# Optimization experiments

Measured on AMD Instinct MI355X. Metric: run time of the kernel, lower is better.

Reference implementation:

```python
import jax, jax.numpy as jnp
import numpy as np

D_MODEL = 2048
NUM_HEADS = 16
D_KV = D_MODEL // NUM_HEADS
THETA = 10000.0
N_LORA = 4
RANK = 16
BATCH = 2
SEQ = 2048


def setup_inputs() -> dict:
    key = jax.random.key(0)
    ks = jax.random.split(key, 16)
    s = 0.02
    inp = {
        'x': jax.random.normal(ks[0], (BATCH, SEQ, D_MODEL), jnp.float32),
        'lora_start_indices': jnp.sort(jax.random.randint(ks[1], (N_LORA,), 0, BATCH)),
        'Wq': jax.random.normal(ks[2], (D_MODEL, D_MODEL), jnp.float32) * s,
        'Aq': jax.random.normal(ks[3], (N_LORA, RANK, D_MODEL), jnp.float32) * s,
        'Bq': jax.random.normal(ks[4], (N_LORA, D_MODEL, RANK), jnp.float32) * s,
        'Wk': jax.random.normal(ks[5], (D_MODEL, D_MODEL), jnp.float32) * s,
        'Ak': jax.random.normal(ks[6], (N_LORA, RANK, D_MODEL), jnp.float32) * s,
        'Bk': jax.random.normal(ks[7], (N_LORA, D_MODEL, RANK), jnp.float32) * s,
        'Wv': jax.random.normal(ks[8], (D_MODEL, D_MODEL), jnp.float32) * s,
        'Av': jax.random.normal(ks[9], (N_LORA, RANK, D_MODEL), jnp.float32) * s,
        'Bv': jax.random.normal(ks[10], (N_LORA, D_MODEL, RANK), jnp.float32) * s,
        'Wo': jax.random.normal(ks[11], (D_MODEL, D_MODEL), jnp.float32) * s,
        'Ao': jax.random.normal(ks[12], (N_LORA, RANK, D_MODEL), jnp.float32) * s,
        'Bo': jax.random.normal(ks[13], (N_LORA, D_MODEL, RANK), jnp.float32) * s,
    }
    return inp


def _adapter_ids(starts, batch):
    # each batch row b uses the adapter whose start index is the last one <= b
    ids = jnp.searchsorted(starts, jnp.arange(batch), side='right') - 1
    return jnp.clip(ids, 0, starts.shape[0] - 1)


def _multilora(x, ids, W, A, B):
    # x: [b, s, d_in]; W: [d_out, d_in]; A: [L, r, d_in]; B: [L, d_out, r]
    base = jnp.einsum('bsd,od->bso', x, W)
    Ai, Bi = A[ids], B[ids]                       # [b, r, d_in], [b, d_out, r]
    low = jnp.einsum('bsd,brd->bsr', x, Ai)
    return base + jnp.einsum('bsr,bor->bso', low, Bi)


def _rope(x):
    # x: [b, h, s, d]; interleaved pair rotation
    d = x.shape[-1]
    pos = jnp.arange(x.shape[-2], dtype=jnp.float32)
    inv_freq = THETA ** (-jnp.arange(0, d, 2, dtype=jnp.float32) / d)  # [d/2]
    ang = pos[:, None] * inv_freq[None, :]                              # [s, d/2]
    cos, sin = jnp.cos(ang), jnp.sin(ang)
    x1, x2 = x[..., 0::2], x[..., 1::2]
    o1 = x1 * cos - x2 * sin
    o2 = x1 * sin + x2 * cos
    return jnp.stack([o1, o2], axis=-1).reshape(x.shape)


def reference(x, lora_start_indices, Wq, Aq, Bq, Wk, Ak, Bk, Wv, Av, Bv, Wo, Ao, Bo):
    b, s, _ = x.shape
    ids = _adapter_ids(lora_start_indices, b)
    Q = _multilora(x, ids, Wq, Aq, Bq)
    K = _multilora(x, ids, Wk, Ak, Bk)
    V = _multilora(x, ids, Wv, Av, Bv)
    # [b, s, h*d] -> [b, h, s, d]
    split = lambda t: t.reshape(b, s, NUM_HEADS, D_KV).transpose(0, 2, 1, 3)
    Q, K, V = split(Q), split(K), split(V)
    Q, K = _rope(Q), _rope(K)
    scores = jnp.einsum('bhqd,bhkd->bhqk', Q, K) / jnp.sqrt(jnp.asarray(D_KV, x.dtype))
    causal = jnp.tril(jnp.ones((s, s), bool))
    scores = jnp.where(causal, scores, jnp.asarray(-jnp.inf, scores.dtype))
    attn = jax.nn.softmax(scores, axis=-1)
    out = jnp.einsum('bhqk,bhkd->bhqd', attn, V)
    out = out.transpose(0, 2, 1, 3).reshape(b, s, D_MODEL)
    return _multilora(out, ids, Wo, Ao, Bo)
```

## Files before the change

### kernel.cpp

```cpp
#include <hip/hip_runtime.h>

typedef unsigned short u16;
typedef unsigned int   u32;
typedef __bf16  bf16x8 __attribute__((ext_vector_type(8)));
typedef float   f32x4  __attribute__((ext_vector_type(4)));

#define D_MODEL 2048
#define SEQ     2048
#define NHEAD   16
#define DKV     128
#define RANK    16

__device__ __forceinline__ u16 f2b(float f) {
  union { float f; u32 i; } v; v.f = f;
  u32 i = v.i;
  return (u16)((i + 0x7FFFu + ((i >> 16) & 1u)) >> 16);
}
__device__ __forceinline__ u32 pack2(float lo, float hi) {
  return (u32)f2b(lo) | ((u32)f2b(hi) << 16);
}
__device__ __forceinline__ float b2f(u16 u) {
  union { u32 i; float f; } v; v.i = ((u32)u) << 16; return v.f;
}
__device__ __forceinline__ float dot2(u32 xa, u32 aa) {
  return b2f((u16)(xa & 0xFFFFu)) * b2f((u16)(aa & 0xFFFFu)) +
         b2f((u16)(xa >> 16))     * b2f((u16)(aa >> 16));
}
__device__ __forceinline__ int adapter_id(const int* starts, int b) {
  int cnt = 0;
#pragma unroll
  for (int i = 0; i < 4; ++i) cnt += (starts[i] <= b) ? 1 : 0;
  int id = cnt - 1;
  return id < 0 ? 0 : (id > 3 ? 3 : id);
}
__device__ __forceinline__ f32x4 mfma16(bf16x8 a, bf16x8 b, f32x4 c) {
  return __builtin_amdgcn_mfma_f32_16x16x32_bf16(a, b, c, 0, 0, 0);
}
__device__ __forceinline__ void gload16(const u16* g, u16* l) {
  __builtin_amdgcn_global_load_lds(
      (const __attribute__((address_space(1))) void*)g,
      (__attribute__((address_space(3))) void*)l, 16, 0, 0);
}

struct CvtArgs {
  const float* src[13];
  u32 base[14];
};
__global__ __launch_bounds__(256) void k_convert(CvtArgs a, u16* __restrict__ dst) {
  const u32 c = blockIdx.x * 256 + threadIdx.x;
  const u32 el0 = c * 8;
  if (el0 >= a.base[13]) return;
  int t = 0;
#pragma unroll
  for (int i = 1; i < 13; ++i) t += (el0 >= a.base[i]) ? 1 : 0;
  const float* s = a.src[t] + (el0 - a.base[t]);
  const float4 lo = *(const float4*)s;
  const float4 hi = *(const float4*)(s + 4);
  uint4 r;
  r.x = pack2(lo.x, lo.y); r.y = pack2(lo.z, lo.w);
  r.z = pack2(hi.x, hi.y); r.w = pack2(hi.z, hi.w);
  *(uint4*)(dst + el0) = r;
}

template <int TAG>
__global__ __launch_bounds__(256) void k_lowrank(
    const u16* __restrict__ X, const u16* __restrict__ A0,
    const u16* __restrict__ A1, const u16* __restrict__ A2,
    const int* __restrict__ starts, float* __restrict__ low, int nout)
{
  const int m = blockIdx.x;
  const int w = threadIdx.x >> 6, lane = threadIdx.x & 63;
  const int id = adapter_id(starts, m >> 11);
  const u16* Xr = X + (size_t)m * D_MODEL;
  for (int o = w; o < nout; o += 4) {
    const int p = o >> 4, r = o & 15;
    const u16* Ar = (p == 0 ? A0 : p == 1 ? A1 : A2) + (size_t)(id * 16 + r) * D_MODEL;
    float sum = 0.f;
#pragma unroll
    for (int c = 0; c < 4; ++c) {
      const int d = c * 512 + lane * 8;
      const uint4 xv = *(const uint4*)(Xr + d);
      const uint4 av = *(const uint4*)(Ar + d);
      sum += dot2(xv.x, av.x) + dot2(xv.y, av.y) + dot2(xv.z, av.z) + dot2(xv.w, av.w);
    }
#pragma unroll
    for (int off = 32; off >= 1; off >>= 1) sum += __shfl_xor(sum, off, 64);
    if (lane == 0) low[(size_t)m * nout + o] = sum;
  }
}

template <int QKV>
__global__ __launch_bounds__(256, 2) void k_gemm(
    const u16* __restrict__ X,
    const u16* __restrict__ W0, const u16* __restrict__ W1, const u16* __restrict__ W2,
    const u16* __restrict__ B0, const u16* __restrict__ B1, const u16* __restrict__ B2,
    const float* __restrict__ low, int ldlow,
    const int* __restrict__ starts,
    u16* __restrict__ D0, u16* __restrict__ D1, u16* __restrict__ D2,
    float* __restrict__ Df)
{
  __shared__ __attribute__((aligned(16))) u16 At[128 * 64];
  __shared__ __attribute__((aligned(16))) u16 Bt[128 * 64];
  const int tid = threadIdx.x;
  const int w = tid >> 6, lane = tid & 63, quad = lane >> 4, l16 = lane & 15;
  const int wr = w >> 1, wc = w & 1;

  const int nwg = gridDim.x * gridDim.y * gridDim.z;
  const int cpx = nwg >> 3;
  const int lin = blockIdx.x + gridDim.x * (blockIdx.y + gridDim.y * blockIdx.z);
  const int nl  = (lin & 7) * cpx + (lin >> 3);
  const int n0 = (nl & 15) * 128, m0 = ((nl >> 4) & 31) * 128, z = nl >> 9;

  const u16* W  = (z == 0) ? W0 : (z == 1) ? W1 : W2;
  const u16* Bm = (z == 0) ? B0 : (z == 1) ? B1 : B2;
  u16*       D  = (z == 0) ? D0 : (z == 1) ? D1 : D2;
  const int loff = QKV ? z * RANK : 0;
  const int id = adapter_id(starts, m0 >> 11);

  const f32x4 zero4 = {0.f, 0.f, 0.f, 0.f};
  f32x4 acc[4][4];
#pragma unroll
  for (int i = 0; i < 4; ++i)
#pragma unroll
    for (int j = 0; j < 4; ++j) acc[i][j] = zero4;

  const int srow_l = lane >> 3;
  const int sgran  = (lane & 7) ^ srow_l;
  const u16* gA = X + (size_t)(m0 + w * 32 + srow_l) * D_MODEL + sgran * 8;
  const u16* gB = W + (size_t)(n0 + w * 32 + srow_l) * D_MODEL + sgran * 8;
  u16* lA = At + (w * 32) * 64;
  u16* lB = Bt + (w * 32) * 64;

  for (int kt = 0; kt < D_MODEL / 64; ++kt) {
    const int kb = kt * 64;
#pragma unroll
    for (int c = 0; c < 4; ++c)
      gload16(gA + (size_t)(c * 8) * D_MODEL + kb, lA + c * 8 * 64);
#pragma unroll
    for (int c = 0; c < 4; ++c)
      gload16(gB + (size_t)(c * 8) * D_MODEL + kb, lB + c * 8 * 64);
    __syncthreads();
#pragma unroll
    for (int kk = 0; kk < 2; ++kk) {
      bf16x8 af[4], bfr[4];
#pragma unroll
      for (int i = 0; i < 4; ++i) {
        const int row = wr * 64 + i * 16 + l16;
        af[i] = *(const bf16x8*)&At[row * 64 + (((kk * 4 + quad) ^ (l16 & 7)) * 8)];
      }
#pragma unroll
      for (int j = 0; j < 4; ++j) {
        const int row = wc * 64 + j * 16 + l16;
        bfr[j] = *(const bf16x8*)&Bt[row * 64 + (((kk * 4 + quad) ^ (l16 & 7)) * 8)];
      }
#pragma unroll
      for (int i = 0; i < 4; ++i)
#pragma unroll
        for (int j = 0; j < 4; ++j)
          acc[i][j] = mfma16(af[i], bfr[j], acc[i][j]);
    }
    __syncthreads();
  }

  for (int e = tid; e < 4096; e += 256) {
    const int rr = e >> 5, kk = e & 31;
    u16 av = 0, bv = 0;
    if (kk < RANK) {
      av = f2b(low[(size_t)(m0 + rr) * ldlow + loff + kk]);
      bv = Bm[((size_t)id * D_MODEL + n0 + rr) * RANK + kk];
    }
    At[rr * 64 + (kk ^ ((rr & 7) << 3))] = av;
    Bt[rr * 64 + (kk ^ ((rr & 7) << 3))] = bv;
  }
  __syncthreads();
  {
    bf16x8 af[4], bfr[4];
#pragma unroll
    for (int i = 0; i < 4; ++i) {
      const int row = wr * 64 + i * 16 + l16;
      af[i] = *(const bf16x8*)&At[row * 64 + ((quad ^ (l16 & 7)) * 8)];
    }
#pragma unroll
    for (int j = 0; j < 4; ++j) {
      const int row = wc * 64 + j * 16 + l16;
      bfr[j] = *(const bf16x8*)&Bt[row * 64 + ((quad ^ (l16 & 7)) * 8)];
    }
#pragma unroll
    for (int i = 0; i < 4; ++i)
#pragma unroll
      for (int j = 0; j < 4; ++j)
        acc[i][j] = mfma16(af[i], bfr[j], acc[i][j]);
  }

  if (QKV) {
    const float scale = (z == 0) ? 0.08838834764831845f : 1.0f;
    const int ropez = (z <= 1);
#pragma unroll
    for (int i = 0; i < 4; ++i) {
      const int mrow = m0 + wr * 64 + i * 16 + quad * 4;
#pragma unroll
      for (int j = 0; j < 4; ++j) {
        const int col = n0 + wc * 64 + j * 16 + l16;
        const int hh = col >> 7, jj = col & (DKV - 1);
        const float invf = exp2f(-0.20762050593046f * (float)(jj >> 1));
#pragma unroll
        for (int r = 0; r < 4; ++r) {
          const int m = mrow + r;
          const int bb = m >> 11, srw = m & (SEQ - 1);
          float v = acc[i][j][r] * scale;
          if (ropez) {
            float sn, cs;
            __sincosf((float)srw * invf, &sn, &cs);
            const float part = __shfl_xor(v, 1, 64);
            v = (jj & 1) ? (part * sn + v * cs) : (v * cs - part * sn);
          }
          D[(((size_t)(bb * NHEAD + hh)) * SEQ + srw) * DKV + jj] = f2b(v);
        }
      }
    }
  } else {
#pragma unroll
    for (int i = 0; i < 4; ++i) {
      const int mrow = m0 + wr * 64 + i * 16 + quad * 4;
#pragma unroll
      for (int j = 0; j < 4; ++j) {
        const int col = n0 + wc * 64 + j * 16 + l16;
#pragma unroll
        for (int r = 0; r < 4; ++r)
          Df[(size_t)(mrow + r) * D_MODEL + col] = acc[i][j][r];
      }
    }
  }
}

#define M0 8.0f
__global__ __launch_bounds__(256, 3) void k_flash(
    const u16* __restrict__ Q, const u16* __restrict__ K,
    const u16* __restrict__ V, u16* __restrict__ O,
    u16* __restrict__ Opart, float* __restrict__ lpart)
{
  __shared__ __attribute__((aligned(16))) u16 Kl[64 * 136];
  __shared__ __attribute__((aligned(16))) u16 VT[DKV * 72];
  __shared__ __attribute__((aligned(16))) u16 Pl[4 * 16 * 72];
  const int tid = threadIdx.x;
  const int w = tid >> 6, lane = tid & 63, quad = lane >> 4, l16 = lane & 15;
  const int lin = blockIdx.x + 32 * blockIdx.y;
  const int nlb = (lin & 7) * 128 + (lin >> 3);
  const int cid = nlb & 31, bh = nlb >> 5;
  const size_t base = (size_t)bh * SEQ * DKV;
  const u16* Qb = Q + base;
  const u16* Kb = K + base;
  const u16* Vb = V + base;
  const int b = bh >> 4, h = bh & 15;
  u16* Plw = &Pl[w * 1152];
  const f32x4 zero4 = {0.f, 0.f, 0.f, 0.f};

  const int dual = (cid < 16);
  const int nA   = dual ? (cid + 1) : 16;
  const int qtB  = 31 - cid;
  const int n    = dual ? 17 : 16;

  const int krr = tid >> 4;
  const int kc8 = (tid & 15) * 8;
  const int vrp = tid & 31;
  const int vcg = tid >> 5;

  int qt = cid, q0 = cid * 64;
  bf16x8 qa[4];
#pragma unroll
  for (int kc = 0; kc < 4; ++kc)
    qa[kc] = *(const bf16x8*)(Qb + (size_t)(q0 + w * 16 + l16) * DKV + kc * 32 + quad * 8);

  f32x4 oacc[8];
#pragma unroll
  for (int nn = 0; nn < 8; ++nn) oacc[nn] = zero4;
  float lr[4] = {0.f, 0.f, 0.f, 0.f};

  uint4 pk[4], pva[2], pvb[2];
#pragma unroll
  for (int it = 0; it < 4; ++it)
    pk[it] = *(const uint4*)(Kb + (size_t)(krr + it * 16) * DKV + kc8);
#pragma unroll
  for (int it = 0; it < 2; ++it) {
    pva[it] = *(const uint4*)(Vb + (size_t)(2 * vrp)     * DKV + (vcg + it * 8) * 8);
    pvb[it] = *(const uint4*)(Vb + (size_t)(2 * vrp + 1) * DKV + (vcg + it * 8) * 8);
  }

  for (int s = 0; s < n; ++s) {
    if (dual && s == nA) {
      float inv[4];
#pragma unroll
      for (int rg = 0; rg < 4; ++rg) {
        float t = lr[rg];
#pragma unroll
        for (int off = 8; off >= 1; off >>= 1) t += __shfl_xor(t, off, 64);
        inv[rg] = 1.f / t;
        lr[rg] = 0.f;
      }
#pragma unroll
      for (int nn = 0; nn < 8; ++nn) {
        const int col = h * DKV + nn * 16 + l16;
#pragma unroll
        for (int rg = 0; rg < 4; ++rg) {
          const int row = q0 + w * 16 + quad * 4 + rg;
          O[((size_t)b * SEQ + row) * D_MODEL + col] = f2b(oacc[nn][rg] * inv[rg]);
        }
#pragma unroll
        for (int e = 0; e < 4; ++e) oacc[nn][e] = 0.f;
      }
      qt = qtB; q0 = qtB * 64;
#pragma unroll
      for (int kc = 0; kc < 4; ++kc)
        qa[kc] = *(const bf16x8*)(Qb + (size_t)(q0 + w * 16 + l16) * DKV + kc * 32 + quad * 8);
    }
    const int kt = (dual && s >= nA) ? (16 + s - nA) : s;

    __syncthreads();
#pragma unroll
    for (int it = 0; it < 4; ++it)
      *(uint4*)(&Kl[(krr + it * 16) * 136 + kc8]) = pk[it];
#pragma unroll
    for (int it = 0; it < 2; ++it) {
      const int c0 = (vcg + it * 8) * 8;
      const uint4 a = pva[it], c = pvb[it];
      *(u32*)&VT[(c0 + 0) * 72 + 2 * vrp] = (a.x & 0xFFFFu) | (c.x << 16);
      *(u32*)&VT[(c0 + 1) * 72 + 2 * vrp] = (a.x >> 16)     | (c.x & 0xFFFF0000u);
      *(u32*)&VT[(c0 + 2) * 72 + 2 * vrp] = (a.y & 0xFFFFu) | (c.y << 16);
      *(u32*)&VT[(c0 + 3) * 72 + 2 * vrp] = (a.y >> 16)     | (c.y & 0xFFFF0000u);
      *(u32*)&VT[(c0 + 4) * 72 + 2 * vrp] = (a.z & 0xFFFFu) | (c.z << 16);
      *(u32*)&VT[(c0 + 5) * 72 + 2 * vrp] = (a.z >> 16)     | (c.z & 0xFFFF0000u);
      *(u32*)&VT[(c0 + 6) * 72 + 2 * vrp] = (a.w & 0xFFFFu) | (c.w << 16);
      *(u32*)&VT[(c0 + 7) * 72 + 2 * vrp] = (a.w >> 16)     | (c.w & 0xFFFF0000u);
    }
    __syncthreads();

    if (s + 1 < n) {
      const int ktn = (dual && (s + 1) >= nA) ? (16 + s + 1 - nA) : (s + 1);
      const size_t ko = (size_t)ktn * 64 * DKV;
#pragma unroll
      for (int it = 0; it < 4; ++it)
        pk[it] = *(const uint4*)(Kb + ko + (size_t)(krr + it * 16) * DKV + kc8);
#pragma unroll
      for (int it = 0; it < 2; ++it) {
        pva[it] = *(const uint4*)(Vb + ko + (size_t)(2 * vrp)     * DKV + (vcg + it * 8) * 8);
        pvb[it] = *(const uint4*)(Vb + ko + (size_t)(2 * vrp + 1) * DKV + (vcg + it * 8) * 8);
      }
    }

    f32x4 sacc[4];
#pragma unroll
    for (int jc = 0; jc < 4; ++jc) sacc[jc] = zero4;
#pragma unroll
    for (int kc = 0; kc < 4; ++kc)
#pragma unroll
      for (int jc = 0; jc < 4; ++jc) {
        const bf16x8 kb = *(const bf16x8*)&Kl[(jc * 16 + l16) * 136 + kc * 32 + quad * 8];
        sacc[jc] = mfma16(qa[kc], kb, sacc[jc]);
      }

    const int diag = (kt == qt);
#pragma unroll
    for (int rg = 0; rg < 4; ++rg) {
      const int qq = q0 + w * 16 + quad * 4 + rg;
      float psum = 0.f;
#pragma unroll
      for (int jc = 0; jc < 4; ++jc) {
        const int kk = kt * 64 + jc * 16 + l16;
        float p = __expf(sacc[jc][rg] - M0);
        if (diag && kk > qq) p = 0.f;
        psum += p;
        Plw[(quad * 4 + rg) * 72 + jc * 16 + l16] = f2b(p);
      }
      lr[rg] += psum;
    }

#pragma unroll
    for (int kc = 0; kc < 2; ++kc) {
      const bf16x8 pa = *(const bf16x8*)&Plw[l16 * 72 + kc * 32 + quad * 8];
#pragma unroll
      for (int nn = 0; nn < 8; ++nn) {
        const bf16x8 vb = *(const bf16x8*)&VT[(nn * 16 + l16) * 72 + kc * 32 + quad * 8];
        oacc[nn] = mfma16(pa, vb, oacc[nn]);
      }
    }
  }

  const int j = dual ? 1 : 0;
  const int slot = (bh * 16 + (qt - 16)) * 2 + j;
#pragma unroll
  for (int rg = 0; rg < 4; ++rg) {
#pragma unroll
    for (int off = 8; off >= 1; off >>= 1) lr[rg] += __shfl_xor(lr[rg], off, 64);
  }
#pragma unroll
  for (int nn = 0; nn < 8; ++nn) {
#pragma unroll
    for (int rg = 0; rg < 4; ++rg) {
      const int row = w * 16 + quad * 4 + rg;
      Opart[(size_t)slot * 8192 + row * 128 + nn * 16 + l16] = f2b(oacc[nn][rg]);
    }
  }
  if (l16 == 0) {
#pragma unroll
    for (int rg = 0; rg < 4; ++rg)
      lpart[slot * 64 + w * 16 + quad * 4 + rg] = lr[rg];
  }
}

__global__ __launch_bounds__(256) void k_merge(
    const u16* __restrict__ Opart, const float* __restrict__ lpart,
    u16* __restrict__ O)
{
  const u32 t = blockIdx.x * 256 + threadIdx.x;
  const u32 u   = t & 63;
  const u32 row = (t >> 6) & 63;
  const u32 q16 = (t >> 12) & 15;
  const u32 bh  = t >> 16;
  const u32 slot0 = (bh * 16 + q16) * 2;
  const u32 o0 = ((slot0 * 8192u + row * 128u) >> 1) + u;
  const u32 a = ((const u32*)Opart)[o0];
  const u32 c = ((const u32*)Opart)[o0 + 4096];
  const float inv = 1.f / (lpart[slot0 * 64 + row] + lpart[(slot0 + 1) * 64 + row]);
  const float r0 = (b2f((u16)(a & 0xFFFFu)) + b2f((u16)(c & 0xFFFFu))) * inv;
  const float r1 = (b2f((u16)(a >> 16))     + b2f((u16)(c >> 16)))     * inv;
  const u32 bb = bh >> 4, h = bh & 15;
  const u32 s = (q16 + 16) * 64 + row;
  ((u32*)O)[(size_t)(bb * SEQ + s) * (D_MODEL / 2) + h * 64 + u] = pack2(r0, r1);
}

extern "C" void kernel_launch(void* const* d_in, const int* in_sizes, int n_in,
                              void* d_out, int out_size, void* d_ws, size_t ws_size,
                              hipStream_t stream) {
  (void)in_sizes; (void)n_in; (void)out_size; (void)ws_size;
  const int* starts = (const int*)d_in[1];

  static const u32 XB = 0;
  static const u32 WQ = 8388608, WK = 12582912, WV = 16777216, WO = 20971520;
  static const u32 AQ = 25165824, AK = 25296896, AV = 25427968, AO = 25559040;
  static const u32 BQ = 25690112, BK = 25821184, BV = 25952256, BO = 26083328;
  static const u32 TOT = 26214400;

  u16* wsb = (u16*)d_ws;
  char* ws = (char*)d_ws;
  float* low_qkv = (float*)(ws + 52428800);
  float* low_o   = (float*)(ws + 53215232);
  u16*   Qb      = (u16*)(ws + 53477376);
  u16*   Kb      = (u16*)(ws + 70254592);
  u16*   Vb      = (u16*)(ws + 87031808);
  u16*   attn    = wsb + XB;
  u16*   Opart   = (u16*)d_out;
  float* lpart   = (float*)((char*)d_out + 16777216);

  CvtArgs ca;
  ca.src[0]  = (const float*)d_in[0];
  ca.src[1]  = (const float*)d_in[2];
  ca.src[2]  = (const float*)d_in[5];
  ca.src[3]  = (const float*)d_in[8];
  ca.src[4]  = (const float*)d_in[11];
  ca.src[5]  = (const float*)d_in[3];
  ca.src[6]  = (const float*)d_in[6];
  ca.src[7]  = (const float*)d_in[9];
  ca.src[8]  = (const float*)d_in[12];
  ca.src[9]  = (const float*)d_in[4];
  ca.src[10] = (const float*)d_in[7];
  ca.src[11] = (const float*)d_in[10];
  ca.src[12] = (const float*)d_in[13];
  const u32 bases[14] = {XB, WQ, WK, WV, WO, AQ, AK, AV, AO, BQ, BK, BV, BO, TOT};
  for (int i = 0; i < 14; ++i) ca.base[i] = bases[i];

  k_convert<<<dim3(TOT / 8 / 256), 256, 0, stream>>>(ca, wsb);

  k_lowrank<0><<<dim3(4096), 256, 0, stream>>>(wsb + XB, wsb + AQ, wsb + AK, wsb + AV,
                                               starts, low_qkv, 48);
  k_gemm<1><<<dim3(16, 32, 3), 256, 0, stream>>>(
      wsb + XB, wsb + WQ, wsb + WK, wsb + WV, wsb + BQ, wsb + BK, wsb + BV,
      low_qkv, 48, starts, Qb, Kb, Vb, (float*)nullptr);
  k_flash<<<dim3(32, 32), 256, 0, stream>>>(Qb, Kb, Vb, attn, Opart, lpart);
  k_merge<<<dim3(8192), 256, 0, stream>>>(Opart, lpart, attn);
  k_lowrank<1><<<dim3(4096), 256, 0, stream>>>(attn, wsb + AO, wsb + AO, wsb + AO,
                                               starts, low_o, 16);
  k_gemm<0><<<dim3(16, 32, 1), 256, 0, stream>>>(
      attn, wsb + WO, wsb + WO, wsb + WO, wsb + BO, wsb + BO, wsb + BO,
      low_o, 16, starts, (u16*)nullptr, (u16*)nullptr, (u16*)nullptr,
      (float*)d_out);
}
```

Measured before the change: 494.2 us.

## Double flash-attention query tile to 128 rows per block for K/V reuse

Result: no change. 490.9 us (-0.7%).

```diff
diff --git a/kernel.cpp b/kernel.cpp
--- a/kernel.cpp
+++ b/kernel.cpp
@@ -234,86 +234,101 @@
 }
 
 #define M0 8.0f
-__global__ __launch_bounds__(256, 3) void k_flash(
+__global__ __launch_bounds__(256, 2) void k_flash(
     const u16* __restrict__ Q, const u16* __restrict__ K,
     const u16* __restrict__ V, u16* __restrict__ O,
     u16* __restrict__ Opart, float* __restrict__ lpart)
 {
   __shared__ __attribute__((aligned(16))) u16 Kl[64 * 136];
   __shared__ __attribute__((aligned(16))) u16 VT[DKV * 72];
-  __shared__ __attribute__((aligned(16))) u16 Pl[4 * 16 * 72];
+  __shared__ __attribute__((aligned(16))) u16 Pl[4 * 32 * 72];
   const int tid = threadIdx.x;
   const int w = tid >> 6, lane = tid & 63, quad = lane >> 4, l16 = lane & 15;
-  const int lin = blockIdx.x + 32 * blockIdx.y;
-  const int nlb = (lin & 7) * 128 + (lin >> 3);
-  const int cid = nlb & 31, bh = nlb >> 5;
+  const int lin = blockIdx.x + 16 * blockIdx.y;
+  const int nlb = (lin & 7) * 64 + (lin >> 3);
+  const int pj = nlb & 15, bh = nlb >> 4;
+  const int pid = pj >> 1, j = pj & 1;
   const size_t base = (size_t)bh * SEQ * DKV;
   const u16* Qb = Q + base;
   const u16* Kb = K + base;
   const u16* Vb = V + base;
   const int b = bh >> 4, h = bh & 15;
-  u16* Plw = &Pl[w * 1152];
+  u16* Plw = &Pl[w * 2304];
   const f32x4 zero4 = {0.f, 0.f, 0.f, 0.f};
 
-  const int dual = (cid < 16);
-  const int nA   = dual ? (cid + 1) : 16;
-  const int qtB  = 31 - cid;
-  const int n    = dual ? 17 : 16;
+  const int qtB = 15 - pid;
+  const int A_steps = (j == 0) ? (2 * pid + 2) : 0;
+  const int kt0 = (j == 0) ? 0 : (15 - 2 * pid);
+
+  int qt = (j == 0) ? pid : qtB;
+  int q0 = qt * 128;
+
+  bf16x8 qa[2][4];
+#pragma unroll
+  for (int h2 = 0; h2 < 2; ++h2)
+#pragma unroll
+    for (int kc = 0; kc < 4; ++kc)
+      qa[h2][kc] = *(const bf16x8*)(Qb + (size_t)(q0 + w * 32 + h2 * 16 + l16) * DKV + kc * 32 + quad * 8);
+
+  f32x4 oacc[2][8];
+#pragma unroll
+  for (int h2 = 0; h2 < 2; ++h2)
+#pragma unroll
+    for (int nn = 0; nn < 8; ++nn) oacc[h2][nn] = zero4;
+  float lr[2][4] = {{0.f,0.f,0.f,0.f},{0.f,0.f,0.f,0.f}};
 
   const int krr = tid >> 4;
   const int kc8 = (tid & 15) * 8;
   const int vrp = tid & 31;
   const int vcg = tid >> 5;
 
-  int qt = cid, q0 = cid * 64;
-  bf16x8 qa[4];
-#pragma unroll
-  for (int kc = 0; kc < 4; ++kc)
-    qa[kc] = *(const bf16x8*)(Qb + (size_t)(q0 + w * 16 + l16) * DKV + kc * 32 + quad * 8);
-
-  f32x4 oacc[8];
-#pragma unroll
-  for (int nn = 0; nn < 8; ++nn) oacc[nn] = zero4;
-  float lr[4] = {0.f, 0.f, 0.f, 0.f};
-
   uint4 pk[4], pva[2], pvb[2];
-#pragma unroll
-  for (int it = 0; it < 4; ++it)
-    pk[it] = *(const uint4*)(Kb + (size_t)(krr + it * 16) * DKV + kc8);
-#pragma unroll
-  for (int it = 0; it < 2; ++it) {
-    pva[it] = *(const uint4*)(Vb + (size_t)(2 * vrp)     * DKV + (vcg + it * 8) * 8);
-    pvb[it] = *(const uint4*)(Vb + (size_t)(2 * vrp + 1) * DKV + (vcg + it * 8) * 8);
-  }
-
-  for (int s = 0; s < n; ++s) {
-    if (dual && s == nA) {
-      float inv[4];
-#pragma unroll
-      for (int rg = 0; rg < 4; ++rg) {
-        float t = lr[rg];
-#pragma unroll
-        for (int off = 8; off >= 1; off >>= 1) t += __shfl_xor(t, off, 64);
-        inv[rg] = 1.f / t;
-        lr[rg] = 0.f;
-      }
-#pragma unroll
-      for (int nn = 0; nn < 8; ++nn) {
-        const int col = h * DKV + nn * 16 + l16;
+  {
+    const size_t ko = (size_t)((j == 0) ? 0 : kt0) * 64 * DKV;
+#pragma unroll
+    for (int it = 0; it < 4; ++it)
+      pk[it] = *(const uint4*)(Kb + ko + (size_t)(krr + it * 16) * DKV + kc8);
+#pragma unroll
+    for (int it = 0; it < 2; ++it) {
+      pva[it] = *(const uint4*)(Vb + ko + (size_t)(2 * vrp)     * DKV + (vcg + it * 8) * 8);
+      pvb[it] = *(const uint4*)(Vb + ko + (size_t)(2 * vrp + 1) * DKV + (vcg + it * 8) * 8);
+    }
+  }
+
+  for (int s = 0; s < 17; ++s) {
+    if (j == 0 && s == A_steps) {
+      float inv[2][4];
+#pragma unroll
+      for (int h2 = 0; h2 < 2; ++h2)
 #pragma unroll
         for (int rg = 0; rg < 4; ++rg) {
-          const int row = q0 + w * 16 + quad * 4 + rg;
-          O[((size_t)b * SEQ + row) * D_MODEL + col] = f2b(oacc[nn][rg] * inv[rg]);
+          float t = lr[h2][rg];
+#pragma unroll
+          for (int off = 8; off >= 1; off >>= 1) t += __shfl_xor(t, off, 64);
+          inv[h2][rg] = 1.f / t;
+          lr[h2][rg] = 0.f;
         }
 #pragma unroll
-        for (int e = 0; e < 4; ++e) oacc[nn][e] = 0.f;
-      }
-      qt = qtB; q0 = qtB * 64;
-#pragma unroll
-      for (int kc = 0; kc < 4; ++kc)
-        qa[kc] = *(const bf16x8*)(Qb + (size_t)(q0 + w * 16 + l16) * DKV + kc * 32 + quad * 8);
-    }
-    const int kt = (dual && s >= nA) ? (16 + s - nA) : s;
+      for (int h2 = 0; h2 < 2; ++h2)
+#pragma unroll
+        for (int nn = 0; nn < 8; ++nn) {
+          const int col = h * DKV + nn * 16 + l16;
+#pragma unroll
+          for (int rg = 0; rg < 4; ++rg) {
+            const int row = q0 + w * 32 + h2 * 16 + quad * 4 + rg;
+            O[((size_t)b * SEQ + row) * D_MODEL + col] = f2b(oacc[h2][nn][rg] * inv[h2][rg]);
+          }
+#pragma unroll
+          for (int e = 0; e < 4; ++e) oacc[h2][nn][e] = 0.f;
+        }
+      qt = qtB; q0 = qt * 128;
+#pragma unroll
+      for (int h2 = 0; h2 < 2; ++h2)
+#pragma unroll
+        for (int kc = 0; kc < 4; ++kc)
+          qa[h2][kc] = *(const bf16x8*)(Qb + (size_t)(q0 + w * 32 + h2 * 16 + l16) * DKV + kc * 32 + quad * 8);
+    }
+    const int kt = (j == 0) ? ((s < A_steps) ? s : s - A_steps) : kt0 + s;
 
     __syncthreads();
 #pragma unroll
@@ -334,8 +349,9 @@
     }
     __syncthreads();
 
-    if (s + 1 < n) {
-      const int ktn = (dual && (s + 1) >= nA) ? (16 + s + 1 - nA) : (s + 1);
+    if (s + 1 < 17) {
+      const int sn = s + 1;
+      const int ktn = (j == 0) ? ((sn < A_steps) ? sn : sn - A_steps) : kt0 + sn;
       const size_t ko = (size_t)ktn * 64 * DKV;
 #pragma unroll
       for (int it = 0; it < 4; ++it)
@@ -347,63 +363,77 @@
       }
     }
 
-    f32x4 sacc[4];
-#pragma unroll
-    for (int jc = 0; jc < 4; ++jc) sacc[jc] = zero4;
+    f32x4 sacc[2][4];
+#pragma unroll
+    for (int h2 = 0; h2 < 2; ++h2)
+#pragma unroll
+      for (int jc = 0; jc < 4; ++jc) sacc[h2][jc] = zero4;
 #pragma unroll
     for (int kc = 0; kc < 4; ++kc)
 #pragma unroll
       for (int jc = 0; jc < 4; ++jc) {
         const bf16x8 kb = *(const bf16x8*)&Kl[(jc * 16 + l16) * 136 + kc * 32 + quad * 8];
-        sacc[jc] = mfma16(qa[kc], kb, sacc[jc]);
-      }
-
-    const int diag = (kt == qt);
-#pragma unroll
-    for (int rg = 0; rg < 4; ++rg) {
-      const int qq = q0 + w * 16 + quad * 4 + rg;
-      float psum = 0.f;
-#pragma unroll
-      for (int jc = 0; jc < 4; ++jc) {
-        const int kk = kt * 64 + jc * 16 + l16;
-        float p = __expf(sacc[jc][rg] - M0);
-        if (diag && kk > qq) p = 0.f;
-        psum += p;
-        Plw[(quad * 4 + rg) * 72 + jc * 16 + l16] = f2b(p);
-      }
-      lr[rg] += psum;
-    }
+        sacc[0][jc] = mfma16(qa[0][kc], kb, sacc[0][jc]);
+        sacc[1][jc] = mfma16(qa[1][kc], kb, sacc[1][jc]);
+      }
+
+    const int diag = (kt >= 2 * qt);
+#pragma unroll
+    for (int h2 = 0; h2 < 2; ++h2)
+#pragma unroll
+      for (int rg = 0; rg < 4; ++rg) {
+        const int qq = q0 + w * 32 + h2 * 16 + quad * 4 + rg;
+        float psum = 0.f;
+#pragma unroll
+        for (int jc = 0; jc < 4; ++jc) {
+          const int kk = kt * 64 + jc * 16 + l16;
+          float p = __expf(sacc[h2][jc][rg] - M0);
+          if (diag && kk > qq) p = 0.f;
+          psum += p;
+          const float pp = __shfl_xor(p, 1, 64);
+          if (!(l16 & 1))
+            *(u32*)&Plw[(h2 * 16 + quad * 4 + rg) * 72 + jc * 16 + l16] = pack2(p, pp);
+        }
+        lr[h2][rg] += psum;
+      }
 
 #pragma unroll
     for (int kc = 0; kc < 2; ++kc) {
-      const bf16x8 pa = *(const bf16x8*)&Plw[l16 * 72 + kc * 32 + quad * 8];
+      const bf16x8 pa0 = *(const bf16x8*)&Plw[(     l16) * 72 + kc * 32 + quad * 8];
+      const bf16x8 pa1 = *(const bf16x8*)&Plw[(16 + l16) * 72 + kc * 32 + quad * 8];
 #pragma unroll
       for (int nn = 0; nn < 8; ++nn) {
         const bf16x8 vb = *(const bf16x8*)&VT[(nn * 16 + l16) * 72 + kc * 32 + quad * 8];
-        oacc[nn] = mfma16(pa, vb, oacc[nn]);
-      }
-    }
-  }
-
-  const int j = dual ? 1 : 0;
-  const int slot = (bh * 16 + (qt - 16)) * 2 + j;
-#pragma unroll
-  for (int rg = 0; rg < 4; ++rg) {
-#pragma unroll
-    for (int off = 8; off >= 1; off >>= 1) lr[rg] += __shfl_xor(lr[rg], off, 64);
-  }
-#pragma unroll
-  for (int nn = 0; nn < 8; ++nn) {
+        oacc[0][nn] = mfma16(pa0, vb, oacc[0][nn]);
+        oacc[1][nn] = mfma16(pa1, vb, oacc[1][nn]);
+      }
+    }
+  }
+
+  const int slot = (bh * 8 + (7 - pid)) * 2 + j;
+#pragma unroll
+  for (int h2 = 0; h2 < 2; ++h2)
 #pragma unroll
     for (int rg = 0; rg < 4; ++rg) {
-      const int row = w * 16 + quad * 4 + rg;
-      Opart[(size_t)slot * 8192 + row * 128 + nn * 16 + l16] = f2b(oacc[nn][rg]);
-    }
-  }
+#pragma unroll
+      for (int off = 8; off >= 1; off >>= 1) lr[h2][rg] += __shfl_xor(lr[h2][rg], off, 64);
+    }
+#pragma unroll
+  for (int h2 = 0; h2 < 2; ++h2)
+#pragma unroll
+    for (int nn = 0; nn < 8; ++nn) {
+#pragma unroll
+      for (int rg = 0; rg < 4; ++rg) {
+        const int row = w * 32 + h2 * 16 + quad * 4 + rg;
+        Opart[(size_t)slot * 16384 + row * 128 + nn * 16 + l16] = f2b(oacc[h2][nn][rg]);
+      }
+    }
   if (l16 == 0) {
 #pragma unroll
-    for (int rg = 0; rg < 4; ++rg)
-      lpart[slot * 64 + w * 16 + quad * 4 + rg] = lr[rg];
+    for (int h2 = 0; h2 < 2; ++h2)
+#pragma unroll
+      for (int rg = 0; rg < 4; ++rg)
+        lpart[slot * 128 + w * 32 + h2 * 16 + quad * 4 + rg] = lr[h2][rg];
   }
 }
 
@@ -413,18 +443,18 @@
 {
   const u32 t = blockIdx.x * 256 + threadIdx.x;
   const u32 u   = t & 63;
-  const u32 row = (t >> 6) & 63;
-  const u32 q16 = (t >> 12) & 15;
+  const u32 row = (t >> 6) & 127;
+  const u32 t8  = (t >> 13) & 7;
   const u32 bh  = t >> 16;
-  const u32 slot0 = (bh * 16 + q16) * 2;
-  const u32 o0 = ((slot0 * 8192u + row * 128u) >> 1) + u;
+  const u32 slot0 = (bh * 8 + t8) * 2;
+  const u32 o0 = slot0 * 8192u + row * 64u + u;
   const u32 a = ((const u32*)Opart)[o0];
-  const u32 c = ((const u32*)Opart)[o0 + 4096];
-  const float inv = 1.f / (lpart[slot0 * 64 + row] + lpart[(slot0 + 1) * 64 + row]);
+  const u32 c = ((const u32*)Opart)[o0 + 8192];
+  const float inv = 1.f / (lpart[slot0 * 128 + row] + lpart[(slot0 + 1) * 128 + row]);
   const float r0 = (b2f((u16)(a & 0xFFFFu)) + b2f((u16)(c & 0xFFFFu))) * inv;
   const float r1 = (b2f((u16)(a >> 16))     + b2f((u16)(c >> 16)))     * inv;
   const u32 bb = bh >> 4, h = bh & 15;
-  const u32 s = (q16 + 16) * 64 + row;
+  const u32 s = (t8 + 8) * 128 + row;
   ((u32*)O)[(size_t)(bb * SEQ + s) * (D_MODEL / 2) + h * 64 + u] = pack2(r0, r1);
 }
 
@@ -475,7 +505,7 @@
   k_gemm<1><<<dim3(16, 32, 3), 256, 0, stream>>>(
       wsb + XB, wsb + WQ, wsb + WK, wsb + WV, wsb + BQ, wsb + BK, wsb + BV,
       low_qkv, 48, starts, Qb, Kb, Vb, (float*)nullptr);
-  k_flash<<<dim3(32, 32), 256, 0, stream>>>(Qb, Kb, Vb, attn, Opart, lpart);
+  k_flash<<<dim3(16, 32), 256, 0, stream>>>(Qb, Kb, Vb, attn, Opart, lpart);
   k_merge<<<dim3(8192), 256, 0, stream>>>(Opart, lpart, attn);
   k_lowrank<1><<<dim3(4096), 256, 0, stream>>>(attn, wsb + AO, wsb + AO, wsb + AO,
                                                starts, low_o, 16);
```
